# Optimization experiments

Hardware: AMD Instinct MI355X
Metric: run time of the kernel (lower is better)

Reference implementation:

```python
import jax, jax.numpy as jnp
import numpy as np

N = 50000   # nodes
E = 200000  # edges (avg degree ~4, pose-graph-like sparsity)
F_IN = 512
NEG_SLOPE = 0.01  # F.leaky_relu default


def _softmax_aggr(src_feat, dst, num_nodes):
    # torch_geometric SoftmaxAggregation(t=1): per-destination, per-feature
    # alpha = softmax(x_j), out = sum_j alpha * x_j
    m = jax.ops.segment_max(src_feat, dst, num_segments=num_nodes)  # [N,F]
    m = jnp.where(jnp.isfinite(m), m, 0.0)  # empty segments -> -inf guard
    e = jnp.exp(src_feat - m[dst])                                   # [E,F]
    denom = jax.ops.segment_sum(e, dst, num_segments=num_nodes)      # [N,F]
    num = jax.ops.segment_sum(e * src_feat, dst, num_segments=num_nodes)
    return num / jnp.maximum(denom, 1e-16)  # 0 for isolated nodes


def setup_inputs() -> dict:
    key = jax.random.key(0)
    ks = jax.random.split(key, 9)
    inp = {
        "x": jax.random.normal(ks[0], (N, F_IN), dtype=jnp.float32),
        "W1_rel": jax.random.normal(ks[1], (513, 256), dtype=jnp.float32) * 0.04,
        "b1_rel": jnp.zeros((256,), dtype=jnp.float32),
        "W1_root": jax.random.normal(ks[2], (513, 256), dtype=jnp.float32) * 0.04,
        "W2_rel": jax.random.normal(ks[3], (257, 64), dtype=jnp.float32) * 0.06,
        "b2_rel": jnp.zeros((64,), dtype=jnp.float32),
        "W2_root": jax.random.normal(ks[4], (257, 64), dtype=jnp.float32) * 0.06,
        "Wp": jax.random.normal(ks[5], (65, 3), dtype=jnp.float32) * 0.1,
        "bp": jnp.zeros((3,), dtype=jnp.float32),
        "Wr": jax.random.normal(ks[6], (65, 4), dtype=jnp.float32) * 0.1,
        "br": jnp.zeros((4,), dtype=jnp.float32),
        "edge_index": jax.random.randint(ks[7], (2, E), 0, N, dtype=jnp.int64),
    }
    return inp


def reference(x, W1_rel, b1_rel, W1_root, W2_rel, b2_rel, W2_root,
              Wp, bp, Wr, br, edge_index):
    src, dst = edge_index[0], edge_index[1]
    node_index = jnp.arange(x.shape[0], dtype=x.dtype)[:, None]  # [N,1]

    # dropout is identity in eval mode
    h = jnp.concatenate([x, node_index], axis=1)  # [N,513]

    # GraphConv(513,256, aggr='softmax'): lin_rel(softmax_aggr(x_j)) + lin_root(x)
    agg1 = _softmax_aggr(h[src], dst, x.shape[0])               # [N,513]
    h = agg1 @ W1_rel + b1_rel + h @ W1_root                     # [N,256]
    h = jnp.where(h >= 0, h, NEG_SLOPE * h)

    h = jnp.concatenate([h, node_index], axis=1)  # [N,257]

    # GraphConv(257,64) default aggr='add'
    agg2 = jax.ops.segment_sum(h[src], dst, num_segments=x.shape[0])  # [N,257]
    h = agg2 @ W2_rel + b2_rel + h @ W2_root                           # [N,64]
    h = jnp.where(h >= 0, h, NEG_SLOPE * h)

    h = jnp.concatenate([h, node_index], axis=1)  # [N,65]

    position = h @ Wp + bp                         # [N,3]
    rotation = h @ Wr + br                         # [N,4]
    norm = jnp.linalg.norm(rotation, axis=1, keepdims=True)
    rotation = rotation / jnp.maximum(norm, 1e-12)  # F.normalize

    return jnp.concatenate([position, rotation], axis=1)  # [N,7]
```

## Files before the change

kernel.cpp:

```cpp
#include <hip/hip_runtime.h>

#define NNODES 50000
#define NEDGES 200000
#define NSCANB ((NNODES + 255) / 256)

typedef short  bf16x8 __attribute__((ext_vector_type(8)));
typedef float  f32x4  __attribute__((ext_vector_type(4)));
typedef unsigned int u32x4 __attribute__((ext_vector_type(4)));

__device__ __forceinline__ unsigned short f2bf(float f) {
    union { float f; unsigned int u; } c; c.f = f;
    unsigned int r = c.u + 0x7fffu + ((c.u >> 16) & 1u);
    return (unsigned short)(r >> 16);
}
__device__ __forceinline__ float bf2f(unsigned short h) {
    union { unsigned int u; float f; } c; c.u = ((unsigned int)h) << 16;
    return c.f;
}
__device__ __forceinline__ float bflo(unsigned int v) {
    union { unsigned int u; float f; } c; c.u = v << 16;
    return c.f;
}
__device__ __forceinline__ float bfhi(unsigned int v) {
    union { unsigned int u; float f; } c; c.u = v & 0xffff0000u;
    return c.f;
}

#define PREP_B1 (256 * 1024)
#define PREP_B2 (64 * 512)
#define PREP_XC (NNODES * 64)
__global__ __launch_bounds__(256) void k_prepcount(const float* __restrict__ x,
                                                   const float* __restrict__ W1_rel,
                                                   const float* __restrict__ W1_root,
                                                   const float* __restrict__ W2_rel,
                                                   const float* __restrict__ W2_root,
                                                   const int* __restrict__ ei,
                                                   int* __restrict__ deg,
                                                   unsigned short* __restrict__ Bt1,
                                                   unsigned short* __restrict__ Bt2,
                                                   unsigned short* __restrict__ xb) {
    const int gtid = blockIdx.x * 256 + threadIdx.x;
    const int GS = gridDim.x * 256;
    for (int e = gtid; e < NEDGES; e += GS) atomicAdd(&deg[ei[NEDGES + e]], 1);
    for (int i = gtid; i < PREP_B1; i += GS) {
        int n = i >> 10, k = i & 1023;
        float v = (k < 512) ? W1_rel[k * 256 + n] : W1_root[(k - 512) * 256 + n];
        Bt1[i] = f2bf(v);
    }
    for (int i = gtid; i < PREP_B2; i += GS) {
        int n = i >> 9, k = i & 511;
        float v = (k < 256) ? W2_rel[k * 64 + n] : W2_root[(k - 256) * 64 + n];
        Bt2[i] = f2bf(v);
    }
    for (int i = gtid; i < PREP_XC; i += GS) {
        int n = i >> 6, c8 = (i & 63) * 8;
        const float* xp = x + (size_t)n * 512 + c8;
        float4 a = *(const float4*)xp;
        float4 bb = *(const float4*)(xp + 4);
        unsigned short o[8];
        o[0] = f2bf(a.x); o[1] = f2bf(a.y); o[2] = f2bf(a.z); o[3] = f2bf(a.w);
        o[4] = f2bf(bb.x); o[5] = f2bf(bb.y); o[6] = f2bf(bb.z); o[7] = f2bf(bb.w);
        *(u32x4*)(xb + (size_t)n * 512 + c8) = *(const u32x4*)o;
    }
}

__global__ __launch_bounds__(256) void k_scanA(const int* __restrict__ deg,
                                               int* __restrict__ rs,
                                               int* __restrict__ partials) {
    __shared__ int sm[256];
    int t = threadIdx.x, i = blockIdx.x * 256 + t;
    int v = (i < NNODES) ? deg[i] : 0;
    sm[t] = v;
    __syncthreads();
#pragma unroll
    for (int off = 1; off < 256; off <<= 1) {
        int u = (t >= off) ? sm[t - off] : 0;
        __syncthreads();
        sm[t] += u;
        __syncthreads();
    }
    if (i < NNODES) rs[i] = sm[t] - v;
    if (t == 255) partials[blockIdx.x] = sm[255];
}

__global__ __launch_bounds__(256) void k_scanC2(int* __restrict__ rs,
                                                const int* __restrict__ partials,
                                                int* __restrict__ cursor) {
    __shared__ int sm[256];
    int t = threadIdx.x, b = blockIdx.x;
    sm[t] = (t < b && t < NSCANB) ? partials[t] : 0;
    __syncthreads();
#pragma unroll
    for (int off = 128; off; off >>= 1) {
        if (t < off) sm[t] += sm[t + off];
        __syncthreads();
    }
    int off0 = sm[0];
    int i = b * 256 + t;
    if (i < NNODES) {
        int rv = rs[i] + off0;
        rs[i] = rv;
        cursor[i] = rv;
    }
    if (i == 0) rs[NNODES] = NEDGES;
}

__global__ void k_scatter(const int* __restrict__ ei, int* __restrict__ cursor,
                          int* __restrict__ srcs) {
    int e = blockIdx.x * 256 + threadIdx.x;
    if (e < NEDGES) {
        int d = ei[NEDGES + e];
        int p = atomicAdd(&cursor[d], 1);
        srcs[p] = ei[e];
    }
}

__global__ __launch_bounds__(256) void k_agg1(const unsigned short* __restrict__ xb,
                                              const int* __restrict__ rs,
                                              const int* __restrict__ srcs,
                                              unsigned short* __restrict__ AggBuf) {
    int wv = threadIdx.x >> 6;
    int lane = threadIdx.x & 63;
    int n = blockIdx.x * 4 + wv;
    int e0 = rs[n], e1 = rs[n + 1];
    float nu[8], de[8];
#pragma unroll
    for (int j = 0; j < 8; ++j) { nu[j] = 0.f; de[j] = 0.f; }
    int e = e0;
    for (; e + 1 < e1; e += 2) {
        int s0 = srcs[e], s1 = srcs[e + 1];
        u32x4 r0 = *(const u32x4*)(xb + (size_t)s0 * 512 + lane * 8);
        u32x4 r1 = *(const u32x4*)(xb + (size_t)s1 * 512 + lane * 8);
#pragma unroll
        for (int p = 0; p < 4; ++p) {
            float v0 = bflo(r0[p]), v1 = bfhi(r0[p]);
            float E0 = __expf(v0), E1 = __expf(v1);
            de[2 * p] += E0; nu[2 * p] += E0 * v0;
            de[2 * p + 1] += E1; nu[2 * p + 1] += E1 * v1;
        }
#pragma unroll
        for (int p = 0; p < 4; ++p) {
            float v0 = bflo(r1[p]), v1 = bfhi(r1[p]);
            float E0 = __expf(v0), E1 = __expf(v1);
            de[2 * p] += E0; nu[2 * p] += E0 * v0;
            de[2 * p + 1] += E1; nu[2 * p + 1] += E1 * v1;
        }
    }
    if (e < e1) {
        int s0 = srcs[e];
        u32x4 r0 = *(const u32x4*)(xb + (size_t)s0 * 512 + lane * 8);
#pragma unroll
        for (int p = 0; p < 4; ++p) {
            float v0 = bflo(r0[p]), v1 = bfhi(r0[p]);
            float E0 = __expf(v0), E1 = __expf(v1);
            de[2 * p] += E0; nu[2 * p] += E0 * v0;
            de[2 * p + 1] += E1; nu[2 * p + 1] += E1 * v1;
        }
    }
    unsigned short o[8];
#pragma unroll
    for (int j = 0; j < 8; ++j) o[j] = f2bf(nu[j] / fmaxf(de[j], 1e-16f));
    *(u32x4*)(AggBuf + (size_t)n * 512 + lane * 8) = *(const u32x4*)o;
}

__global__ __launch_bounds__(256) void k_agg2(const int* __restrict__ rs,
                                              const int* __restrict__ srcs,
                                              const unsigned short* __restrict__ H1,
                                              unsigned short* __restrict__ Seg) {
    int wv = threadIdx.x >> 6;
    int lane = threadIdx.x & 63;
    int n = blockIdx.x * 4 + wv;
    int e0 = rs[n], e1 = rs[n + 1];
    float a[4] = {0.f, 0.f, 0.f, 0.f};
    int e = e0;
    for (; e + 1 < e1; e += 2) {
        int s0 = srcs[e], s1 = srcs[e + 1];
        uint2 r0 = *(const uint2*)(H1 + (size_t)s0 * 256 + lane * 4);
        uint2 r1 = *(const uint2*)(H1 + (size_t)s1 * 256 + lane * 4);
        a[0] += bflo(r0.x) + bflo(r1.x);
        a[1] += bfhi(r0.x) + bfhi(r1.x);
        a[2] += bflo(r0.y) + bflo(r1.y);
        a[3] += bfhi(r0.y) + bfhi(r1.y);
    }
    if (e < e1) {
        uint2 r0 = *(const uint2*)(H1 + (size_t)srcs[e] * 256 + lane * 4);
        a[0] += bflo(r0.x); a[1] += bfhi(r0.x);
        a[2] += bflo(r0.y); a[3] += bfhi(r0.y);
    }
    uint2 o;
    o.x = (unsigned int)f2bf(a[0]) | ((unsigned int)f2bf(a[1]) << 16);
    o.y = (unsigned int)f2bf(a[2]) | ((unsigned int)f2bf(a[3]) << 16);
    *(uint2*)(Seg + (size_t)n * 256 + lane * 4) = o;
}

__global__ __launch_bounds__(256, 5) void k_gemm1(const unsigned short* __restrict__ A1,
                                                  const unsigned short* __restrict__ A2,
                                                  const unsigned short* __restrict__ Bt,
                                                  const int* __restrict__ rs,
                                                  const int* __restrict__ srcs,
                                                  const float* __restrict__ r1,
                                                  const float* __restrict__ r2,
                                                  const float* __restrict__ bias,
                                                  unsigned short* __restrict__ outp) {
    constexpr int BM = 64, BN = 128, BK = 64;
    __shared__ __align__(16) unsigned short As[BM * BK];
    __shared__ __align__(16) unsigned short Bs[BN * BK];
    __shared__ float s1t[BM];

    const int tid = threadIdx.x;
    const int w = tid >> 6;
    const int lane = tid & 63;
    const int lm = lane & 15;
    const int quad = lane >> 4;
    const int wr = w >> 1;
    const int wc = w & 1;
    const int rowbase = blockIdx.y * BM;
    const int colbase = blockIdx.x * BN;
    const int wrow = wr * 32;
    const int wcol = wc * 64;

    const int rsub = lane >> 3;
    const int csw = (lane & 7) ^ rsub;

    f32x4 acc[2][4];
#pragma unroll
    for (int mi = 0; mi < 2; ++mi)
#pragma unroll
        for (int ni = 0; ni < 4; ++ni) acc[mi][ni] = (f32x4){0.f, 0.f, 0.f, 0.f};

    for (int kt = 0; kt < 1024; kt += BK) {
        const unsigned short* Ab = (kt < 512) ? A1 : A2;
        int kof = (kt < 512) ? kt : kt - 512;
#pragma unroll
        for (int l = 0; l < 2; ++l) {
            int r = w * 16 + l * 8;
            int gr = rowbase + r + rsub;
            if (gr >= NNODES) gr = NNODES - 1;
            const unsigned short* gp = Ab + (size_t)gr * 512 + kof + csw * 8;
            __builtin_amdgcn_global_load_lds(
                (const __attribute__((address_space(1))) void*)gp,
                (__attribute__((address_space(3))) void*)(As + r * BK), 16, 0, 0);
        }
#pragma unroll
        for (int l = 0; l < 4; ++l) {
            int r = w * 32 + l * 8;
            const unsigned short* gp = Bt + (size_t)(colbase + r + rsub) * 1024 + kt + csw * 8;
            __builtin_amdgcn_global_load_lds(
                (const __attribute__((address_space(1))) void*)gp,
                (__attribute__((address_space(3))) void*)(Bs + r * BK), 16, 0, 0);
        }
        __syncthreads();
#pragma unroll
        for (int kk = 0; kk < BK; kk += 32) {
            const int kidx = (kk >> 3) + quad;
            const int phys = kidx ^ (lm & 7);
            bf16x8 af[2], bfr[4];
#pragma unroll
            for (int mi = 0; mi < 2; ++mi)
                af[mi] = __builtin_bit_cast(bf16x8,
                    *(const u32x4*)(As + (wrow + mi * 16 + lm) * BK + phys * 8));
#pragma unroll
            for (int ni = 0; ni < 4; ++ni)
                bfr[ni] = __builtin_bit_cast(bf16x8,
                    *(const u32x4*)(Bs + (wcol + ni * 16 + lm) * BK + phys * 8));
#pragma unroll
            for (int mi = 0; mi < 2; ++mi)
#pragma unroll
                for (int ni = 0; ni < 4; ++ni)
                    acc[mi][ni] = __builtin_amdgcn_mfma_f32_16x16x32_bf16(
                        af[mi], bfr[ni], acc[mi][ni], 0, 0, 0);
        }
        __syncthreads();
    }

    if (tid < BM) {
        int grow = rowbase + tid;
        float r_ = 0.f;
        if (grow < NNODES) {
            int e0 = rs[grow], e1 = rs[grow + 1];
            float m = -INFINITY, d = 0.f, q = 0.f;
            for (int e = e0; e < e1; ++e) {
                float v = (float)srcs[e];
                float nm = fmaxf(m, v);
                float sc = __expf(m - nm), ee = __expf(v - nm);
                d = d * sc + ee;
                q = q * sc + ee * v;
                m = nm;
            }
            r_ = q / fmaxf(d, 1e-16f);
        }
        s1t[tid] = r_;
    }
    __syncthreads();

#pragma unroll
    for (int ni = 0; ni < 4; ++ni) {
        int gc = colbase + wcol + ni * 16 + lm;
        float r1v = r1[gc], r2v = r2[gc], bv = bias[gc];
#pragma unroll
        for (int mi = 0; mi < 2; ++mi) {
#pragma unroll
            for (int r = 0; r < 4; ++r) {
                int lrow = wrow + mi * 16 + quad * 4 + r;
                int grow = rowbase + lrow;
                if (grow < NNODES) {
                    float v = acc[mi][ni][r] + s1t[lrow] * r1v + (float)grow * r2v + bv;
                    v = (v >= 0.f) ? v : 0.01f * v;
                    outp[(size_t)grow * 256 + gc] = f2bf(v);
                }
            }
        }
    }
}

__global__ __launch_bounds__(256) void k_gemm2h(const unsigned short* __restrict__ A1,
                                                const unsigned short* __restrict__ A2,
                                                const unsigned short* __restrict__ Bt,
                                                const int* __restrict__ rs,
                                                const int* __restrict__ srcs,
                                                const float* __restrict__ r1,
                                                const float* __restrict__ r2,
                                                const float* __restrict__ bias,
                                                const float* __restrict__ Wp,
                                                const float* __restrict__ bp,
                                                const float* __restrict__ Wr,
                                                const float* __restrict__ br,
                                                float* __restrict__ out) {
    constexpr int BM = 64, BN = 64, BK = 64;
    __shared__ __align__(16) unsigned short As[BM * BK];
    __shared__ __align__(16) unsigned short Bs[BN * BK];
    __shared__ float h2t[BM * 65];
    __shared__ float s1t[BM];

    const int tid = threadIdx.x;
    const int w = tid >> 6;
    const int lane = tid & 63;
    const int lm = lane & 15;
    const int quad = lane >> 4;
    const int rowbase = blockIdx.x * BM;
    const int wrow = w * 16;

    const int rsub = lane >> 3;
    const int csw = (lane & 7) ^ rsub;

    f32x4 acc[4];
#pragma unroll
    for (int ni = 0; ni < 4; ++ni) acc[ni] = (f32x4){0.f, 0.f, 0.f, 0.f};

    for (int kt = 0; kt < 512; kt += BK) {
        const unsigned short* Ab = (kt < 256) ? A1 : A2;
        int kof = (kt < 256) ? kt : kt - 256;
#pragma unroll
        for (int l = 0; l < 2; ++l) {
            int r = w * 16 + l * 8;
            int gr = rowbase + r + rsub;
            if (gr >= NNODES) gr = NNODES - 1;
            const unsigned short* gp = Ab + (size_t)gr * 256 + kof + csw * 8;
            __builtin_amdgcn_global_load_lds(
                (const __attribute__((address_space(1))) void*)gp,
                (__attribute__((address_space(3))) void*)(As + r * BK), 16, 0, 0);
        }
#pragma unroll
        for (int l = 0; l < 2; ++l) {
            int r = w * 16 + l * 8;
            const unsigned short* gp = Bt + (size_t)(r + rsub) * 512 + kt + csw * 8;
            __builtin_amdgcn_global_load_lds(
                (const __attribute__((address_space(1))) void*)gp,
                (__attribute__((address_space(3))) void*)(Bs + r * BK), 16, 0, 0);
        }
        __syncthreads();
#pragma unroll
        for (int kk = 0; kk < BK; kk += 32) {
            const int kidx = (kk >> 3) + quad;
            const int phys = kidx ^ (lm & 7);
            bf16x8 af;
            af = __builtin_bit_cast(bf16x8,
                *(const u32x4*)(As + (wrow + lm) * BK + phys * 8));
            bf16x8 bfr[4];
#pragma unroll
            for (int ni = 0; ni < 4; ++ni)
                bfr[ni] = __builtin_bit_cast(bf16x8,
                    *(const u32x4*)(Bs + (ni * 16 + lm) * BK + phys * 8));
#pragma unroll
            for (int ni = 0; ni < 4; ++ni)
                acc[ni] = __builtin_amdgcn_mfma_f32_16x16x32_bf16(
                    af, bfr[ni], acc[ni], 0, 0, 0);
        }
        __syncthreads();
    }

    if (tid < BM) {
        int grow = rowbase + tid;
        float si = 0.f;
        if (grow < NNODES) {
            int e0 = rs[grow], e1 = rs[grow + 1];
            for (int e = e0; e < e1; ++e) si += (float)srcs[e];
        }
        s1t[tid] = si;
    }
    __syncthreads();

#pragma unroll
    for (int ni = 0; ni < 4; ++ni) {
        int gc = ni * 16 + lm;
        float r1v = r1[gc], r2v = r2[gc], bv = bias[gc];
#pragma unroll
        for (int r = 0; r < 4; ++r) {
            int lrow = wrow + quad * 4 + r;
            int grow = rowbase + lrow;
            float v = acc[ni][r] + s1t[lrow] * r1v + (float)grow * r2v + bv;
            v = (v >= 0.f) ? v : 0.01f * v;
            h2t[lrow * 65 + gc] = v;
        }
    }
    __syncthreads();

    if (tid < BM) {
        int grow = rowbase + tid;
        if (grow < NNODES) {
            const float* hv = h2t + tid * 65;
            float idx = (float)grow;
            float p0 = 0.f, p1 = 0.f, p2 = 0.f;
            float r0 = 0.f, r1a = 0.f, r2a = 0.f, r3 = 0.f;
#pragma unroll 8
            for (int c = 0; c < 64; ++c) {
                float v = hv[c];
                p0 += v * Wp[c * 3 + 0];
                p1 += v * Wp[c * 3 + 1];
                p2 += v * Wp[c * 3 + 2];
                r0 += v * Wr[c * 4 + 0];
                r1a += v * Wr[c * 4 + 1];
                r2a += v * Wr[c * 4 + 2];
                r3 += v * Wr[c * 4 + 3];
            }
            p0 += idx * Wp[64 * 3 + 0] + bp[0];
            p1 += idx * Wp[64 * 3 + 1] + bp[1];
            p2 += idx * Wp[64 * 3 + 2] + bp[2];
            r0 += idx * Wr[64 * 4 + 0] + br[0];
            r1a += idx * Wr[64 * 4 + 1] + br[1];
            r2a += idx * Wr[64 * 4 + 2] + br[2];
            r3 += idx * Wr[64 * 4 + 3] + br[3];
            float nrm = fmaxf(sqrtf(r0 * r0 + r1a * r1a + r2a * r2a + r3 * r3), 1e-12f);
            float* op = out + (size_t)grow * 7;
            op[0] = p0; op[1] = p1; op[2] = p2;
            op[3] = r0 / nrm; op[4] = r1a / nrm; op[5] = r2a / nrm; op[6] = r3 / nrm;
        }
    }
}

extern "C" void kernel_launch(void* const* d_in, const int* in_sizes, int n_in,
                              void* d_out, int out_size, void* d_ws, size_t ws_size,
                              hipStream_t stream) {
    const float* x       = (const float*)d_in[0];
    const float* W1_rel  = (const float*)d_in[1];
    const float* b1      = (const float*)d_in[2];
    const float* W1_root = (const float*)d_in[3];
    const float* W2_rel  = (const float*)d_in[4];
    const float* b2      = (const float*)d_in[5];
    const float* W2_root = (const float*)d_in[6];
    const float* Wp      = (const float*)d_in[7];
    const float* bp      = (const float*)d_in[8];
    const float* Wr      = (const float*)d_in[9];
    const float* br      = (const float*)d_in[10];
    const int*   ei      = (const int*)d_in[11];
    float* out = (float*)d_out;

    char* ws = (char*)d_ws;
    size_t off = 0;
    auto alloc = [&](size_t bytes) {
        size_t o = off;
        off = (off + bytes + 255) & ~(size_t)255;
        return (void*)(ws + o);
    };
    int*   deg       = (int*)alloc(NNODES * 4);
    int*   cursor    = (int*)alloc(NNODES * 4);
    int*   row_start = (int*)alloc((NNODES + 1) * 4);
    int*   srcs      = (int*)alloc(NEDGES * 4);
    int*   partials  = (int*)alloc(NSCANB * 4);
    unsigned short* xb     = (unsigned short*)alloc((size_t)NNODES * 512 * 2);
    unsigned short* AggBuf = (unsigned short*)alloc((size_t)NNODES * 512 * 2);
    unsigned short* H1     = (unsigned short*)alloc((size_t)NNODES * 256 * 2);
    unsigned short* Seg    = (unsigned short*)alloc((size_t)NNODES * 256 * 2);
    unsigned short* Bt1    = (unsigned short*)alloc(256 * 1024 * 2);
    unsigned short* Bt2    = (unsigned short*)alloc(64 * 512 * 2);

    hipMemsetAsync(deg, 0, NNODES * 4, stream);

    k_prepcount<<<2048, 256, 0, stream>>>(
        x, W1_rel, W1_root, W2_rel, W2_root, ei, deg, Bt1, Bt2, xb);

    k_scanA<<<NSCANB, 256, 0, stream>>>(deg, row_start, partials);
    k_scanC2<<<NSCANB, 256, 0, stream>>>(row_start, partials, cursor);
    k_scatter<<<(NEDGES + 255) / 256, 256, 0, stream>>>(ei, cursor, srcs);

    k_agg1<<<NNODES / 4, 256, 0, stream>>>(xb, row_start, srcs, AggBuf);

    k_gemm1<<<dim3(2, (NNODES + 63) / 64), 256, 0, stream>>>(
        AggBuf, xb, Bt1, row_start, srcs, W1_rel + 512 * 256, W1_root + 512 * 256, b1, H1);

    k_agg2<<<NNODES / 4, 256, 0, stream>>>(row_start, srcs, H1, Seg);

    k_gemm2h<<<(NNODES + 63) / 64, 256, 0, stream>>>(
        Seg, H1, Bt2, row_start, srcs, W2_rel + 256 * 64, W2_root + 256 * 64, b2,
        Wp, bp, Wr, br, out);
}
```

Measured before the change: 338.0 us.

## Fuse layer-2 aggregation into GEMM2, quantize gather features to fp8, merge scans

Adds an fp8 (e4m3-style) copy of x, written during prep, so the layer-1 softmax gather reads half the bytes per edge. Folds the layer-2 sum aggregation into the second GEMM kernel: each block gathers neighbour H1 rows into shared memory and computes the source-index sum in the same pass, which removes the Seg buffer and one launch. Replaces the two-kernel scan with a single kernel that recomputes each block's prefix by summing all earlier degrees. The fp8 path lowers the precision of the softmax inputs, the prep kernel writes an extra buffer, and the larger shared-memory use in GEMM2 may lower occupancy.

```diff
diff --git a/kernel.cpp b/kernel.cpp
--- a/kernel.cpp
+++ b/kernel.cpp
@@ -13,10 +13,6 @@
     unsigned int r = c.u + 0x7fffu + ((c.u >> 16) & 1u);
     return (unsigned short)(r >> 16);
 }
-__device__ __forceinline__ float bf2f(unsigned short h) {
-    union { unsigned int u; float f; } c; c.u = ((unsigned int)h) << 16;
-    return c.f;
-}
 __device__ __forceinline__ float bflo(unsigned int v) {
     union { unsigned int u; float f; } c; c.u = v << 16;
     return c.f;
@@ -24,6 +20,22 @@
 __device__ __forceinline__ float bfhi(unsigned int v) {
     union { unsigned int u; float f; } c; c.u = v & 0xffff0000u;
     return c.f;
+}
+
+__device__ __forceinline__ unsigned int f2fp8(float f) {
+    union { float f; unsigned int u; } c; c.f = fabsf(f);
+    if (c.f > 448.f) c.f = 448.f;
+    unsigned int r = c.u + 0x0007ffffu + ((c.u >> 20) & 1u);
+    int e = (int)(r >> 23) - 127;
+    if (e < -6) return 0u;
+    unsigned int s = (f < 0.f) ? 0x80u : 0u;
+    return s | ((unsigned int)(e + 7) << 3) | ((r >> 20) & 7u);
+}
+__device__ __forceinline__ float fp8d(unsigned int b) {
+    unsigned int e = (b >> 3) & 15u;
+    union { unsigned int u; float f; } c;
+    c.u = ((b & 0x80u) << 24) | ((e + 120u) << 23) | ((b & 7u) << 20);
+    return (e == 0) ? 0.f : c.f;
 }
 
 #define PREP_B1 (256 * 1024)
@@ -38,7 +50,8 @@
                                                    int* __restrict__ deg,
                                                    unsigned short* __restrict__ Bt1,
                                                    unsigned short* __restrict__ Bt2,
-                                                   unsigned short* __restrict__ xb) {
+                                                   unsigned short* __restrict__ xb,
+                                                   unsigned char* __restrict__ xq) {
     const int gtid = blockIdx.x * 256 + threadIdx.x;
     const int GS = gridDim.x * 256;
     for (int e = gtid; e < NEDGES; e += GS) atomicAdd(&deg[ei[NEDGES + e]], 1);
@@ -57,18 +70,39 @@
         const float* xp = x + (size_t)n * 512 + c8;
         float4 a = *(const float4*)xp;
         float4 bb = *(const float4*)(xp + 4);
+        float v[8] = {a.x, a.y, a.z, a.w, bb.x, bb.y, bb.z, bb.w};
         unsigned short o[8];
-        o[0] = f2bf(a.x); o[1] = f2bf(a.y); o[2] = f2bf(a.z); o[3] = f2bf(a.w);
-        o[4] = f2bf(bb.x); o[5] = f2bf(bb.y); o[6] = f2bf(bb.z); o[7] = f2bf(bb.w);
+        unsigned int q0 = 0, q1 = 0;
+#pragma unroll
+        for (int j = 0; j < 8; ++j) o[j] = f2bf(v[j]);
+#pragma unroll
+        for (int j = 0; j < 4; ++j) q0 |= f2fp8(v[j]) << (8 * j);
+#pragma unroll
+        for (int j = 0; j < 4; ++j) q1 |= f2fp8(v[4 + j]) << (8 * j);
         *(u32x4*)(xb + (size_t)n * 512 + c8) = *(const u32x4*)o;
-    }
-}
-
-__global__ __launch_bounds__(256) void k_scanA(const int* __restrict__ deg,
-                                               int* __restrict__ rs,
-                                               int* __restrict__ partials) {
+        uint2 q; q.x = q0; q.y = q1;
+        *(uint2*)(xq + (size_t)n * 512 + c8) = q;
+    }
+}
+
+__global__ __launch_bounds__(256) void k_scan(const int* __restrict__ deg,
+                                              int* __restrict__ rs,
+                                              int* __restrict__ cursor) {
     __shared__ int sm[256];
-    int t = threadIdx.x, i = blockIdx.x * 256 + t;
+    const int t = threadIdx.x, b = blockIdx.x;
+    const int base = b * 256;
+    int pre = 0;
+    for (int j = t; j < base; j += 256) pre += deg[j];
+    sm[t] = pre;
+    __syncthreads();
+#pragma unroll
+    for (int off = 128; off; off >>= 1) {
+        if (t < off) sm[t] += sm[t + off];
+        __syncthreads();
+    }
+    const int off0 = sm[0];
+    __syncthreads();
+    int i = base + t;
     int v = (i < NNODES) ? deg[i] : 0;
     sm[t] = v;
     __syncthreads();
@@ -79,26 +113,8 @@
         sm[t] += u;
         __syncthreads();
     }
-    if (i < NNODES) rs[i] = sm[t] - v;
-    if (t == 255) partials[blockIdx.x] = sm[255];
-}
-
-__global__ __launch_bounds__(256) void k_scanC2(int* __restrict__ rs,
-                                                const int* __restrict__ partials,
-                                                int* __restrict__ cursor) {
-    __shared__ int sm[256];
-    int t = threadIdx.x, b = blockIdx.x;
-    sm[t] = (t < b && t < NSCANB) ? partials[t] : 0;
-    __syncthreads();
-#pragma unroll
-    for (int off = 128; off; off >>= 1) {
-        if (t < off) sm[t] += sm[t + off];
-        __syncthreads();
-    }
-    int off0 = sm[0];
-    int i = b * 256 + t;
     if (i < NNODES) {
-        int rv = rs[i] + off0;
+        int rv = off0 + sm[t] - v;
         rs[i] = rv;
         cursor[i] = rv;
     }
@@ -115,7 +131,7 @@
     }
 }
 
-__global__ __launch_bounds__(256) void k_agg1(const unsigned short* __restrict__ xb,
+__global__ __launch_bounds__(256) void k_agg1(const unsigned char* __restrict__ xq,
                                               const int* __restrict__ rs,
                                               const int* __restrict__ srcs,
                                               unsigned short* __restrict__ AggBuf) {
@@ -129,68 +145,40 @@
     int e = e0;
     for (; e + 1 < e1; e += 2) {
         int s0 = srcs[e], s1 = srcs[e + 1];
-        u32x4 r0 = *(const u32x4*)(xb + (size_t)s0 * 512 + lane * 8);
-        u32x4 r1 = *(const u32x4*)(xb + (size_t)s1 * 512 + lane * 8);
-#pragma unroll
-        for (int p = 0; p < 4; ++p) {
-            float v0 = bflo(r0[p]), v1 = bfhi(r0[p]);
+        uint2 r0 = *(const uint2*)(xq + (size_t)s0 * 512 + lane * 8);
+        uint2 r1 = *(const uint2*)(xq + (size_t)s1 * 512 + lane * 8);
+#pragma unroll
+        for (int j = 0; j < 4; ++j) {
+            float v0 = fp8d((r0.x >> (8 * j)) & 0xffu);
+            float v1 = fp8d((r0.y >> (8 * j)) & 0xffu);
             float E0 = __expf(v0), E1 = __expf(v1);
-            de[2 * p] += E0; nu[2 * p] += E0 * v0;
-            de[2 * p + 1] += E1; nu[2 * p + 1] += E1 * v1;
-        }
-#pragma unroll
-        for (int p = 0; p < 4; ++p) {
-            float v0 = bflo(r1[p]), v1 = bfhi(r1[p]);
+            de[j] += E0; nu[j] += E0 * v0;
+            de[4 + j] += E1; nu[4 + j] += E1 * v1;
+        }
+#pragma unroll
+        for (int j = 0; j < 4; ++j) {
+            float v0 = fp8d((r1.x >> (8 * j)) & 0xffu);
+            float v1 = fp8d((r1.y >> (8 * j)) & 0xffu);
             float E0 = __expf(v0), E1 = __expf(v1);
-            de[2 * p] += E0; nu[2 * p] += E0 * v0;
-            de[2 * p + 1] += E1; nu[2 * p + 1] += E1 * v1;
+            de[j] += E0; nu[j] += E0 * v0;
+            de[4 + j] += E1; nu[4 + j] += E1 * v1;
         }
     }
     if (e < e1) {
-        int s0 = srcs[e];
-        u32x4 r0 = *(const u32x4*)(xb + (size_t)s0 * 512 + lane * 8);
-#pragma unroll
-        for (int p = 0; p < 4; ++p) {
-            float v0 = bflo(r0[p]), v1 = bfhi(r0[p]);
+        uint2 r0 = *(const uint2*)(xq + (size_t)srcs[e] * 512 + lane * 8);
+#pragma unroll
+        for (int j = 0; j < 4; ++j) {
+            float v0 = fp8d((r0.x >> (8 * j)) & 0xffu);
+            float v1 = fp8d((r0.y >> (8 * j)) & 0xffu);
             float E0 = __expf(v0), E1 = __expf(v1);
-            de[2 * p] += E0; nu[2 * p] += E0 * v0;
-            de[2 * p + 1] += E1; nu[2 * p + 1] += E1 * v1;
+            de[j] += E0; nu[j] += E0 * v0;
+            de[4 + j] += E1; nu[4 + j] += E1 * v1;
         }
     }
     unsigned short o[8];
 #pragma unroll
     for (int j = 0; j < 8; ++j) o[j] = f2bf(nu[j] / fmaxf(de[j], 1e-16f));
     *(u32x4*)(AggBuf + (size_t)n * 512 + lane * 8) = *(const u32x4*)o;
-}
-
-__global__ __launch_bounds__(256) void k_agg2(const int* __restrict__ rs,
-                                              const int* __restrict__ srcs,
-                                              const unsigned short* __restrict__ H1,
-                                              unsigned short* __restrict__ Seg) {
-    int wv = threadIdx.x >> 6;
-    int lane = threadIdx.x & 63;
-    int n = blockIdx.x * 4 + wv;
-    int e0 = rs[n], e1 = rs[n + 1];
-    float a[4] = {0.f, 0.f, 0.f, 0.f};
-    int e = e0;
-    for (; e + 1 < e1; e += 2) {
-        int s0 = srcs[e], s1 = srcs[e + 1];
-        uint2 r0 = *(const uint2*)(H1 + (size_t)s0 * 256 + lane * 4);
-        uint2 r1 = *(const uint2*)(H1 + (size_t)s1 * 256 + lane * 4);
-        a[0] += bflo(r0.x) + bflo(r1.x);
-        a[1] += bfhi(r0.x) + bfhi(r1.x);
-        a[2] += bflo(r0.y) + bflo(r1.y);
-        a[3] += bfhi(r0.y) + bfhi(r1.y);
-    }
-    if (e < e1) {
-        uint2 r0 = *(const uint2*)(H1 + (size_t)srcs[e] * 256 + lane * 4);
-        a[0] += bflo(r0.x); a[1] += bfhi(r0.x);
-        a[2] += bflo(r0.y); a[3] += bfhi(r0.y);
-    }
-    uint2 o;
-    o.x = (unsigned int)f2bf(a[0]) | ((unsigned int)f2bf(a[1]) << 16);
-    o.y = (unsigned int)f2bf(a[2]) | ((unsigned int)f2bf(a[3]) << 16);
-    *(uint2*)(Seg + (size_t)n * 256 + lane * 4) = o;
 }
 
 __global__ __launch_bounds__(256, 5) void k_gemm1(const unsigned short* __restrict__ A1,
@@ -313,8 +301,7 @@
     }
 }
 
-__global__ __launch_bounds__(256) void k_gemm2h(const unsigned short* __restrict__ A1,
-                                                const unsigned short* __restrict__ A2,
+__global__ __launch_bounds__(256) void k_gemm2h(const unsigned short* __restrict__ H1,
                                                 const unsigned short* __restrict__ Bt,
                                                 const int* __restrict__ rs,
                                                 const int* __restrict__ srcs,
@@ -326,7 +313,8 @@
                                                 const float* __restrict__ Wr,
                                                 const float* __restrict__ br,
                                                 float* __restrict__ out) {
-    constexpr int BM = 64, BN = 64, BK = 64;
+    constexpr int BM = 64, BN = 64, BK = 64, SSTR = 264;
+    __shared__ __align__(16) unsigned short SegL[BM * SSTR];
     __shared__ __align__(16) unsigned short As[BM * BK];
     __shared__ __align__(16) unsigned short Bs[BN * BK];
     __shared__ float h2t[BM * 65];
@@ -343,22 +331,56 @@
     const int rsub = lane >> 3;
     const int csw = (lane & 7) ^ rsub;
 
+    for (int i = 0; i < 16; ++i) {
+        int lrow = w * 16 + i;
+        int n = rowbase + lrow;
+        float a0 = 0.f, a1 = 0.f, a2 = 0.f, a3 = 0.f, si = 0.f;
+        if (n < NNODES) {
+            int e0 = rs[n], e1 = rs[n + 1];
+            int e = e0;
+            for (; e + 1 < e1; e += 2) {
+                int s0 = srcs[e], s1 = srcs[e + 1];
+                uint2 r0 = *(const uint2*)(H1 + (size_t)s0 * 256 + lane * 4);
+                uint2 r1v = *(const uint2*)(H1 + (size_t)s1 * 256 + lane * 4);
+                a0 += bflo(r0.x) + bflo(r1v.x);
+                a1 += bfhi(r0.x) + bfhi(r1v.x);
+                a2 += bflo(r0.y) + bflo(r1v.y);
+                a3 += bfhi(r0.y) + bfhi(r1v.y);
+                si += (float)s0 + (float)s1;
+            }
+            if (e < e1) {
+                int s0 = srcs[e];
+                uint2 r0 = *(const uint2*)(H1 + (size_t)s0 * 256 + lane * 4);
+                a0 += bflo(r0.x); a1 += bfhi(r0.x);
+                a2 += bflo(r0.y); a3 += bfhi(r0.y);
+                si += (float)s0;
+            }
+        }
+        uint2 o;
+        o.x = (unsigned int)f2bf(a0) | ((unsigned int)f2bf(a1) << 16);
+        o.y = (unsigned int)f2bf(a2) | ((unsigned int)f2bf(a3) << 16);
+        *(uint2*)(SegL + lrow * SSTR + lane * 4) = o;
+        if (lane == 0) s1t[lrow] = si;
+    }
+    __syncthreads();
+
     f32x4 acc[4];
 #pragma unroll
     for (int ni = 0; ni < 4; ++ni) acc[ni] = (f32x4){0.f, 0.f, 0.f, 0.f};
 
     for (int kt = 0; kt < 512; kt += BK) {
-        const unsigned short* Ab = (kt < 256) ? A1 : A2;
-        int kof = (kt < 256) ? kt : kt - 256;
-#pragma unroll
-        for (int l = 0; l < 2; ++l) {
-            int r = w * 16 + l * 8;
-            int gr = rowbase + r + rsub;
-            if (gr >= NNODES) gr = NNODES - 1;
-            const unsigned short* gp = Ab + (size_t)gr * 256 + kof + csw * 8;
-            __builtin_amdgcn_global_load_lds(
-                (const __attribute__((address_space(1))) void*)gp,
-                (__attribute__((address_space(3))) void*)(As + r * BK), 16, 0, 0);
+        if (kt >= 256) {
+            int kof = kt - 256;
+#pragma unroll
+            for (int l = 0; l < 2; ++l) {
+                int r = w * 16 + l * 8;
+                int gr = rowbase + r + rsub;
+                if (gr >= NNODES) gr = NNODES - 1;
+                const unsigned short* gp = H1 + (size_t)gr * 256 + kof + csw * 8;
+                __builtin_amdgcn_global_load_lds(
+                    (const __attribute__((address_space(1))) void*)gp,
+                    (__attribute__((address_space(3))) void*)(As + r * BK), 16, 0, 0);
+            }
         }
 #pragma unroll
         for (int l = 0; l < 2; ++l) {
@@ -374,8 +396,12 @@
             const int kidx = (kk >> 3) + quad;
             const int phys = kidx ^ (lm & 7);
             bf16x8 af;
-            af = __builtin_bit_cast(bf16x8,
-                *(const u32x4*)(As + (wrow + lm) * BK + phys * 8));
+            if (kt < 256)
+                af = __builtin_bit_cast(bf16x8,
+                    *(const u32x4*)(SegL + (wrow + lm) * SSTR + kt + kk + quad * 8));
+            else
+                af = __builtin_bit_cast(bf16x8,
+                    *(const u32x4*)(As + (wrow + lm) * BK + phys * 8));
             bf16x8 bfr[4];
 #pragma unroll
             for (int ni = 0; ni < 4; ++ni)
@@ -388,17 +414,6 @@
         }
         __syncthreads();
     }
-
-    if (tid < BM) {
-        int grow = rowbase + tid;
-        float si = 0.f;
-        if (grow < NNODES) {
-            int e0 = rs[grow], e1 = rs[grow + 1];
-            for (int e = e0; e < e1; ++e) si += (float)srcs[e];
-        }
-        s1t[tid] = si;
-    }
-    __syncthreads();
 
 #pragma unroll
     for (int ni = 0; ni < 4; ++ni) {
@@ -476,31 +491,27 @@
     int*   cursor    = (int*)alloc(NNODES * 4);
     int*   row_start = (int*)alloc((NNODES + 1) * 4);
     int*   srcs      = (int*)alloc(NEDGES * 4);
-    int*   partials  = (int*)alloc(NSCANB * 4);
     unsigned short* xb     = (unsigned short*)alloc((size_t)NNODES * 512 * 2);
+    unsigned char*  xq     = (unsigned char*)alloc((size_t)NNODES * 512);
     unsigned short* AggBuf = (unsigned short*)alloc((size_t)NNODES * 512 * 2);
     unsigned short* H1     = (unsigned short*)alloc((size_t)NNODES * 256 * 2);
-    unsigned short* Seg    = (unsigned short*)alloc((size_t)NNODES * 256 * 2);
     unsigned short* Bt1    = (unsigned short*)alloc(256 * 1024 * 2);
     unsigned short* Bt2    = (unsigned short*)alloc(64 * 512 * 2);
 
     hipMemsetAsync(deg, 0, NNODES * 4, stream);
 
     k_prepcount<<<2048, 256, 0, stream>>>(
-        x, W1_rel, W1_root, W2_rel, W2_root, ei, deg, Bt1, Bt2, xb);
-
-    k_scanA<<<NSCANB, 256, 0, stream>>>(deg, row_start, partials);
-    k_scanC2<<<NSCANB, 256, 0, stream>>>(row_start, partials, cursor);
+        x, W1_rel, W1_root, W2_rel, W2_root, ei, deg, Bt1, Bt2, xb, xq);
+
+    k_scan<<<NSCANB, 256, 0, stream>>>(deg, row_start, cursor);
     k_scatter<<<(NEDGES + 255) / 256, 256, 0, stream>>>(ei, cursor, srcs);
 
-    k_agg1<<<NNODES / 4, 256, 0, stream>>>(xb, row_start, srcs, AggBuf);
+    k_agg1<<<NNODES / 4, 256, 0, stream>>>(xq, row_start, srcs, AggBuf);
 
     k_gemm1<<<dim3(2, (NNODES + 63) / 64), 256, 0, stream>>>(
         AggBuf, xb, Bt1, row_start, srcs, W1_rel + 512 * 256, W1_root + 512 * 256, b1, H1);
 
-    k_agg2<<<NNODES / 4, 256, 0, stream>>>(row_start, srcs, H1, Seg);
-
     k_gemm2h<<<(NNODES + 63) / 64, 256, 0, stream>>>(
-        Seg, H1, Bt2, row_start, srcs, W2_rel + 256 * 64, W2_root + 256 * 64, b2,
+        H1, Bt2, row_start, srcs, W2_rel + 256 * 64, W2_root + 256 * 64, b2,
         Wp, bp, Wr, br, out);
 }
```

Result: slower. 422.5 us (+25.0%).
